# Kernel optimization log

Measured on AMD Instinct MI355X. Metric: run time of the kernel, lower is better.

## Reference

```python
import jax, jax.numpy as jnp
import numpy as np

EMBED = 512
HEADS = 8
HEAD_DIM = EMBED // HEADS
SCALE_BASE = 512
NEG = -1e9


def xpos_apply(x, offset, downscale):
    # x: [(b h), L, d]
    L, d = x.shape[1], x.shape[2]
    min_pos = -(L + offset) // 2
    max_pos = L + offset + min_pos
    base = (jnp.arange(0, d, 2, dtype=jnp.float32) + 0.4 * d) / (1.4 * d)      # [d/2]
    power = jnp.arange(min_pos, max_pos, dtype=jnp.float32) / SCALE_BASE        # [L']
    scale = base[None, :] ** power[:, None]                                     # [L', d/2]
    half = d // 2
    inv_freq = 1.0 / (10000.0 ** (jnp.arange(half, dtype=jnp.float32) / half))
    sinusoid = jnp.arange(scale.shape[0], dtype=jnp.float32)[:, None] * inv_freq[None, :]
    sin, cos = jnp.sin(sinusoid), jnp.cos(sinusoid)
    # keep last L rows (no-op when offset == 0)
    scale, sin, cos = scale[-L:], sin[-L:], cos[-L:]
    if downscale:
        scale = 1.0 / scale
    sin2 = jnp.repeat(sin * scale, 2, axis=-1)   # duplicate_interleave -> [L, d]
    cos2 = jnp.repeat(cos * scale, 2, axis=-1)
    x1, x2 = x[..., ::2], x[..., 1::2]
    rot = jnp.stack([-x2, x1], axis=-1).reshape(x.shape)  # rotate_every_two
    return x * cos2[None] + rot * sin2[None]


def split_heads(x, b, L):
    # 'b l (h d) -> (b h) l d'
    return x.reshape(b, L, HEADS, HEAD_DIM).transpose(0, 2, 1, 3).reshape(b * HEADS, L, HEAD_DIM)


def setup_inputs() -> dict:
    key = jax.random.key(0)
    ks = jax.random.split(key, 12)
    b, L = 4, 2048
    inp = {
        'query': jax.random.normal(ks[0], (b, L, EMBED), jnp.float32),
        'key': jax.random.normal(ks[1], (b, L, EMBED), jnp.float32),
        'value': jax.random.normal(ks[2], (b, L, EMBED), jnp.float32),
        'key_padding_mask': jnp.zeros((b, L), jnp.bool_),
        'attn_mask': jnp.where(jnp.tril(jnp.ones((L, L), jnp.bool_)), 0.0, NEG).astype(jnp.float32),
    }
    s = 1.0 / np.sqrt(EMBED)
    inp['Wq'] = jax.random.normal(ks[3], (EMBED, EMBED), jnp.float32) * s
    inp['bq'] = jnp.zeros((EMBED,), jnp.float32)
    inp['Wk'] = jax.random.normal(ks[4], (EMBED, EMBED), jnp.float32) * s
    inp['bk'] = jnp.zeros((EMBED,), jnp.float32)
    inp['Wv'] = jax.random.normal(ks[5], (EMBED, EMBED), jnp.float32) * s
    inp['bv'] = jnp.zeros((EMBED,), jnp.float32)
    inp['Wo'] = jax.random.normal(ks[6], (EMBED, EMBED), jnp.float32) * s
    inp['bo'] = jnp.zeros((EMBED,), jnp.float32)
    return inp


def reference(query, key, value, key_padding_mask, attn_mask, Wq, bq, Wk, bk, Wv, bv, Wo, bo):
    b, L, _ = query.shape
    q = split_heads(query @ Wq.T + bq, b, L)
    k = split_heads(key @ Wk.T + bk, b, L)
    v = split_heads(value @ Wv.T + bv, b, L)
    k = xpos_apply(k, 0, True)
    q = xpos_apply(q, 0, False)
    q = q * (HEAD_DIM ** -0.5)
    aw = jnp.einsum('btd,bsd->bts', q, k)                 # [(b h), t, s]
    aw = jnp.nan_to_num(aw) + attn_mask[None]
    aw = aw.reshape(b, HEADS, L, L)
    aw = jnp.where(key_padding_mask[:, None, None, :], jnp.finfo(aw.dtype).min, aw)
    aw = aw.reshape(b * HEADS, L, L)
    probs = jax.nn.softmax(aw.astype(jnp.float32), axis=-1).astype(aw.dtype)
    attn = jnp.einsum('bts,bsd->btd', probs, v)           # [(b h), t, d]
    attn = attn.reshape(b, HEADS, L, HEAD_DIM).transpose(0, 2, 1, 3).reshape(b, L, EMBED)
    return attn @ Wo.T + bo
```

## Files before the change

### kernel.cpp

```cpp
#include <hip/hip_runtime.h>
#include <hip/hip_bf16.h>

typedef __bf16 bf16x2 __attribute__((ext_vector_type(2)));
typedef __bf16 bf16x4 __attribute__((ext_vector_type(4)));
typedef __bf16 bf16x8 __attribute__((ext_vector_type(8)));
typedef float  f32x4  __attribute__((ext_vector_type(4)));

#define SEQ    2048
#define EMB    512
#define NHEAD  8
#define HD     64
#define NBATCH 4
#define MROWS  (NBATCH*SEQ)
#define QSCALE 0.18033688011112042f
#define INV2PI 0.15915494309189535f
#define TWOPI  6.28318530717958648f
#define NEGFREQ (-0.41524101186092028f)

__device__ __forceinline__ f32x4 mfma16(bf16x8 a, bf16x8 b, f32x4 c) {
  return __builtin_amdgcn_mfma_f32_16x16x32_bf16(a, b, c, 0, 0, 0);
}

typedef __attribute__((address_space(1))) const void gv_t;
typedef __attribute__((address_space(3))) void lv_t;
__device__ __forceinline__ void async16(const void* g, void* l) {
  __builtin_amdgcn_global_load_lds((gv_t*)g, (lv_t*)l, 16, 0, 0);
}

__global__ __launch_bounds__(256) void conv_kernel(const float* __restrict__ q,
                                                   const float* __restrict__ k,
                                                   const float* __restrict__ v,
                                                   __bf16* __restrict__ Qf,
                                                   __bf16* __restrict__ Kf,
                                                   __bf16* __restrict__ Vf) {
  const int z = blockIdx.y;
  const float* src = (z == 0) ? q : (z == 1) ? k : v;
  __bf16* dst = (z == 0) ? Qf : (z == 1) ? Kf : Vf;
  const size_t i8 = ((size_t)blockIdx.x * 256 + threadIdx.x) * 8;
  const float4 fa = ((const float4*)(src + i8))[0];
  const float4 fb = ((const float4*)(src + i8))[1];
  bf16x8 h = { (__bf16)fa.x, (__bf16)fa.y, (__bf16)fa.z, (__bf16)fa.w,
               (__bf16)fb.x, (__bf16)fb.y, (__bf16)fb.z, (__bf16)fb.w };
  *(bf16x8*)(dst + i8) = h;
}

__global__ __launch_bounds__(256) void convw_kernel(const float* __restrict__ wq,
                                                    const float* __restrict__ wk,
                                                    const float* __restrict__ wv,
                                                    const float* __restrict__ wo,
                                                    __bf16* __restrict__ Wb) {
  const int z = blockIdx.x >> 7;
  const float* src = (z == 0) ? wq : (z == 1) ? wk : (z == 2) ? wv : wo;
  __bf16* dst = Wb + (size_t)z * (EMB * EMB);
  const size_t i8 = ((size_t)(blockIdx.x & 127) * 256 + threadIdx.x) * 8;
  const float4 fa = ((const float4*)(src + i8))[0];
  const float4 fb = ((const float4*)(src + i8))[1];
  bf16x8 h = { (__bf16)fa.x, (__bf16)fa.y, (__bf16)fa.z, (__bf16)fa.w,
               (__bf16)fb.x, (__bf16)fb.y, (__bf16)fb.z, (__bf16)fb.w };
  *(bf16x8*)(dst + i8) = h;
}

__device__ __forceinline__ void gemm_main(const __bf16* __restrict__ A,
                                          const __bf16* __restrict__ W,
                                          __bf16* As, __bf16* Bs,
                                          f32x4 (&acc)[4][4], int m0, int n0) {
  const int tid = threadIdx.x;
  const int wid = tid >> 6, lane = tid & 63;
  const int quad = lane >> 4, l16 = lane & 15;
  const int l7 = l16 & 7;
  const int srow = lane >> 3;
  const int sxor = ((lane & 7) ^ srow) * 8;
  const int wm = (wid >> 1) * 64, wn = (wid & 1) * 64;

  #pragma unroll
  for (int i = 0; i < 4; ++i)
    #pragma unroll
    for (int j = 0; j < 4; ++j) acc[i][j] = (f32x4)(0.0f);

  for (int k0 = 0; k0 < 512; k0 += 64) {
    __syncthreads();
    #pragma unroll
    for (int ii = 0; ii < 4; ++ii) {
      const int r8 = wid * 32 + ii * 8;
      async16(A + (size_t)(m0 + r8 + srow) * 512 + k0 + sxor, &As[r8 * 64]);
      async16(W + (size_t)(n0 + r8 + srow) * 512 + k0 + sxor, &Bs[r8 * 64]);
    }
    __syncthreads();
    #pragma unroll
    for (int ks = 0; ks < 2; ++ks) {
      bf16x8 af[4], bfr[4];
      #pragma unroll
      for (int i = 0; i < 4; ++i)
        af[i] = *(const bf16x8*)&As[(wm + i * 16 + l16) * 64 +
                                    (((quad + ks * 4) ^ l7) * 8)];
      #pragma unroll
      for (int j = 0; j < 4; ++j)
        bfr[j] = *(const bf16x8*)&Bs[(wn + j * 16 + l16) * 64 +
                                     (((quad + ks * 4) ^ l7) * 8)];
      #pragma unroll
      for (int i = 0; i < 4; ++i)
        #pragma unroll
        for (int j = 0; j < 4; ++j)
          acc[i][j] = mfma16(af[i], bfr[j], acc[i][j]);
    }
  }
}

__global__ __launch_bounds__(256) void gemm_proj_kernel(
    const __bf16* __restrict__ Qf, const __bf16* __restrict__ Kf, const __bf16* __restrict__ Vf,
    const __bf16* __restrict__ Wb,
    const float* __restrict__ bq, const float* __restrict__ bk, const float* __restrict__ bv,
    __bf16* __restrict__ Qx, __bf16* __restrict__ Kx, __bf16* __restrict__ Vt) {
  __shared__ __align__(16) char smem[34816];
  __bf16* As = (__bf16*)smem;
  __bf16* Bs = (__bf16*)(smem + 16384);
  __bf16* T  = (__bf16*)smem;

  const int z = blockIdx.z;
  const __bf16* A = (z == 0) ? Qf : (z == 1) ? Kf : Vf;
  const __bf16* W = Wb + (size_t)z * (EMB * EMB);
  const float* bias = (z == 0) ? bq : (z == 1) ? bk : bv;
  const int m0 = blockIdx.y * 128, n0 = blockIdx.x * 128;

  f32x4 acc[4][4];
  gemm_main(A, W, As, Bs, acc, m0, n0);

  const int tid = threadIdx.x;
  const int wid = tid >> 6, lane = tid & 63;
  const int quad = lane >> 4, l16 = lane & 15;
  const int wm = (wid >> 1) * 64, wn = (wid & 1) * 64;

  __syncthreads();

  if (z == 2) {
    #pragma unroll
    for (int j = 0; j < 4; ++j) {
      const float bval = bias[n0 + wn + j * 16 + l16];
      #pragma unroll
      for (int i = 0; i < 4; ++i) {
        bf16x4 p = { (__bf16)(acc[i][j][0] + bval), (__bf16)(acc[i][j][1] + bval),
                     (__bf16)(acc[i][j][2] + bval), (__bf16)(acc[i][j][3] + bval) };
        *(bf16x4*)&T[(wn + j * 16 + l16) * 136 + wm + i * 16 + quad * 4] = p;
      }
    }
    __syncthreads();
    const int nrow = tid >> 1, mh = (tid & 1) << 6;
    bf16x8 vv[8];
    #pragma unroll
    for (int u = 0; u < 8; ++u) vv[u] = *(const bf16x8*)&T[nrow * 136 + mh + u * 8];
    const int n = n0 + nrow, h = n >> 6, d = n & 63;
    const int bb = m0 >> 11, lb2 = (m0 & 2047) + mh;
    __bf16* dst = Vt + ((size_t)(bb * 8 + h) * 64 + d) * 2048 + lb2;
    #pragma unroll
    for (int u = 0; u < 8; ++u) *(bf16x8*)(dst + u * 8) = vv[u];
  } else {
    #pragma unroll
    for (int j = 0; j < 4; ++j) {
      const float bval = bias[n0 + wn + j * 16 + l16];
      #pragma unroll
      for (int i = 0; i < 4; ++i)
        #pragma unroll
        for (int r = 0; r < 4; ++r)
          T[(wm + i * 16 + quad * 4 + r) * 136 + wn + j * 16 + l16] =
              (__bf16)(acc[i][j][r] + bval);
    }
    __syncthreads();
    const int lrow = tid >> 1, half = tid & 1;
    const int gm = m0 + lrow, l = gm & 2047, bb = gm >> 11;
    const int h = (n0 >> 6) + half;
    bf16x8 vv[8];
    #pragma unroll
    for (int u = 0; u < 8; ++u)
      vv[u] = *(const bf16x8*)&T[lrow * 136 + half * 64 + u * 8];
    bf16x8 ov[8];
    const float lf = (float)l;
    const float pw = (lf - 1024.0f) * (1.0f / 512.0f);
    const float qs = (z == 0) ? QSCALE : 1.0f;
    #pragma unroll
    for (int i = 0; i < 32; ++i) {
      const float x1 = (float)vv[i >> 2][(2 * i) & 7];
      const float x2 = (float)vv[i >> 2][(2 * i + 1) & 7];
      const float lb = __log2f((2.0f * i + 25.6f) * (1.0f / 89.6f));
      const float e  = (z == 0) ? (pw * lb) : (-pw * lb);
      const float sc = __builtin_amdgcn_exp2f(e) * qs;
      const float ang = lf * __builtin_amdgcn_exp2f((float)i * NEGFREQ);
      float rev = ang * INV2PI;
      rev -= floorf(rev);
      const float ar = rev * TWOPI;
      const float sn = __sinf(ar) * sc;
      const float cs = __cosf(ar) * sc;
      ov[i >> 2][(2 * i) & 7]     = (__bf16)(x1 * cs - x2 * sn);
      ov[i >> 2][(2 * i + 1) & 7] = (__bf16)(x2 * cs + x1 * sn);
    }
    __bf16* dst = ((z == 0) ? Qx : Kx) + ((size_t)(bb * 8 + h) * 2048 + l) * 64;
    #pragma unroll
    for (int u = 0; u < 8; ++u) *(bf16x8*)(dst + u * 8) = ov[u];
  }
}

__global__ __launch_bounds__(256) void gemm_out_kernel(
    const __bf16* __restrict__ A, const __bf16* __restrict__ W,
    const float* __restrict__ bias, float* __restrict__ C) {
  __shared__ __align__(16) char smem[34816];
  __bf16* As = (__bf16*)smem;
  __bf16* Bs = (__bf16*)(smem + 16384);
  const int m0 = blockIdx.y * 128, n0 = blockIdx.x * 128;
  f32x4 acc[4][4];
  gemm_main(A, W, As, Bs, acc, m0, n0);
  const int tid = threadIdx.x;
  const int wid = tid >> 6, lane = tid & 63;
  const int quad = lane >> 4, l16 = lane & 15;
  const int wm = (wid >> 1) * 64, wn = (wid & 1) * 64;
  #pragma unroll
  for (int j = 0; j < 4; ++j) {
    const int n = n0 + wn + j * 16 + l16;
    const float bval = bias[n];
    #pragma unroll
    for (int i = 0; i < 4; ++i)
      #pragma unroll
      for (int r = 0; r < 4; ++r)
        C[(size_t)(m0 + wm + i * 16 + quad * 4 + r) * 512 + n] = acc[i][j][r] + bval;
  }
}

__global__ __launch_bounds__(256) void flash_kernel(const __bf16* __restrict__ Qx,
                                                    const __bf16* __restrict__ Kx,
                                                    const __bf16* __restrict__ Vt,
                                                    const unsigned char* __restrict__ kpm,
                                                    __bf16* __restrict__ Oa) {
  __shared__ __align__(16) __bf16 Ks[2][64 * HD];
  __shared__ __align__(16) __bf16 Vs[2][64 * HD];
  __shared__ __align__(16) __bf16 Qs[64 * HD];

  const int tid = threadIdx.x;
  const int wid = tid >> 6;
  const int lane = tid & 63;
  const int quad = lane >> 4;
  const int l16 = lane & 15;
  const int l7 = l16 & 7;
  const int srow = lane >> 3;
  const int sxor = ((lane & 7) ^ srow) * 8;
  const int bh = blockIdx.x;
  const int b = bh >> 3;
  const int qb = 31 - (int)blockIdx.y;
  const int q0 = qb * 64;

  const __bf16* Qbase = Qx + (size_t)bh * (SEQ * HD);
  const __bf16* Kbase = Kx + (size_t)bh * (SEQ * HD);
  const __bf16* Vbase = Vt + (size_t)bh * (HD * SEQ);
  __bf16* Pw = Qs + wid * 1024;

  #pragma unroll
  for (int ii = 0; ii < 2; ++ii) {
    const int r0 = wid * 16 + ii * 8;
    async16(Qbase + (size_t)(q0 + r0 + srow) * HD + sxor, &Qs[r0 * HD]);
    async16(Kbase + (size_t)(r0 + srow) * HD + sxor, &Ks[0][r0 * HD]);
    async16(Vbase + (size_t)(r0 + srow) * SEQ + sxor, &Vs[0][r0 * HD]);
  }
  __syncthreads();
  const bf16x8 qf0 = *(const bf16x8*)&Qs[(wid * 16 + l16) * HD + ((quad ^ l7) * 8)];
  const bf16x8 qf1 = *(const bf16x8*)&Qs[(wid * 16 + l16) * HD + (((quad + 4) ^ l7) * 8)];

  f32x4 o0 = (f32x4)(0.0f), o1 = (f32x4)(0.0f), o2 = (f32x4)(0.0f), o3 = (f32x4)(0.0f);
  float m_run = -1e30f, l_run = 0.0f;
  const int myq = q0 + wid * 16 + l16;
  const int niter = qb + 1;

  for (int it = 0; it < niter; ++it) {
    const int kv0 = it << 6;
    const int cur = it & 1;
    const __bf16* Kc = &Ks[cur][0];
    const __bf16* Vc = &Vs[cur][0];

    if (it + 1 < niter) {
      const int kn = kv0 + 64;
      #pragma unroll
      for (int ii = 0; ii < 2; ++ii) {
        const int r0 = wid * 16 + ii * 8;
        async16(Kbase + (size_t)(kn + r0 + srow) * HD + sxor, &Ks[cur ^ 1][r0 * HD]);
        async16(Vbase + (size_t)(r0 + srow) * SEQ + kn + sxor, &Vs[cur ^ 1][r0 * HD]);
      }
    }
    const unsigned char* kp0 = kpm + b * SEQ + kv0;
    unsigned pk[4];
    #pragma unroll
    for (int nb = 0; nb < 4; ++nb)
      pk[nb] = *(const unsigned*)(kp0 + nb * 16 + quad * 4);

    f32x4 s[4];
    #pragma unroll
    for (int nb = 0; nb < 4; ++nb) s[nb] = (f32x4)(0.0f);
    __builtin_amdgcn_s_setprio(1);
    #pragma unroll
    for (int nb = 0; nb < 4; ++nb) {
      const bf16x8 kf = *(const bf16x8*)&Kc[(nb * 16 + l16) * HD + ((quad ^ l7) * 8)];
      s[nb] = mfma16(kf, qf0, s[nb]);
    }
    #pragma unroll
    for (int nb = 0; nb < 4; ++nb) {
      const bf16x8 kf = *(const bf16x8*)&Kc[(nb * 16 + l16) * HD + (((quad + 4) ^ l7) * 8)];
      s[nb] = mfma16(kf, qf1, s[nb]);
    }
    __builtin_amdgcn_s_setprio(0);

    if (kv0 + 63 > q0 + wid * 16) {
      #pragma unroll
      for (int nb = 0; nb < 4; ++nb)
        #pragma unroll
        for (int r = 0; r < 4; ++r)
          if (kv0 + nb * 16 + quad * 4 + r > myq) s[nb][r] = -1e30f;
    }
    #pragma unroll
    for (int nb = 0; nb < 4; ++nb) {
      if (pk[nb]) {
        if (pk[nb] & 0x000000FFu) s[nb][0] = -1e30f;
        if (pk[nb] & 0x0000FF00u) s[nb][1] = -1e30f;
        if (pk[nb] & 0x00FF0000u) s[nb][2] = -1e30f;
        if (pk[nb] & 0xFF000000u) s[nb][3] = -1e30f;
      }
    }

    float mx;
    {
      f32x4 u0, u1;
      #pragma unroll
      for (int r = 0; r < 4; ++r) u0[r] = fmaxf(s[0][r], s[1][r]);
      #pragma unroll
      for (int r = 0; r < 4; ++r) u1[r] = fmaxf(s[2][r], s[3][r]);
      #pragma unroll
      for (int r = 0; r < 4; ++r) u0[r] = fmaxf(u0[r], u1[r]);
      mx = fmaxf(fmaxf(u0[0], u0[1]), fmaxf(u0[2], u0[3]));
    }
    mx = fmaxf(mx, __shfl_xor(mx, 16));
    mx = fmaxf(mx, __shfl_xor(mx, 32));
    if (__any(mx > m_run)) {
      const float m_new = fmaxf(m_run, mx);
      const float alpha = __builtin_amdgcn_exp2f(m_run - m_new);
      o0 *= alpha; o1 *= alpha; o2 *= alpha; o3 *= alpha;
      l_run *= alpha;
      m_run = m_new;
    }
    #pragma unroll
    for (int nb = 0; nb < 4; ++nb)
      #pragma unroll
      for (int r = 0; r < 4; ++r)
        s[nb][r] = __builtin_amdgcn_exp2f(s[nb][r] - m_run);
    {
      f32x4 v01 = s[0] + s[1];
      f32x4 v23 = s[2] + s[3];
      f32x4 vt = v01 + v23;
      float ssum = (vt[0] + vt[1]) + (vt[2] + vt[3]);
      ssum += __shfl_xor(ssum, 16);
      ssum += __shfl_xor(ssum, 32);
      l_run += ssum;
    }

    #pragma unroll
    for (int nb = 0; nb < 4; ++nb) {
      bf16x4 p4 = { (__bf16)s[nb][0], (__bf16)s[nb][1],
                    (__bf16)s[nb][2], (__bf16)s[nb][3] };
      *(bf16x4*)&Pw[l16 * 64 + (((nb * 2 + (quad >> 1)) ^ l7) << 3) + (quad & 1) * 4] = p4;
    }

    __builtin_amdgcn_s_setprio(1);
    #pragma unroll
    for (int ks = 0; ks < 2; ++ks) {
      const bf16x8 pf = *(const bf16x8*)&Pw[l16 * 64 + (((ks * 4 + quad) ^ l7) << 3)];
      const int bx = ((quad + ks * 4) ^ l7) * 8;
      o0 = mfma16(*(const bf16x8*)&Vc[( 0 + l16) * HD + bx], pf, o0);
      o1 = mfma16(*(const bf16x8*)&Vc[(16 + l16) * HD + bx], pf, o1);
      o2 = mfma16(*(const bf16x8*)&Vc[(32 + l16) * HD + bx], pf, o2);
      o3 = mfma16(*(const bf16x8*)&Vc[(48 + l16) * HD + bx], pf, o3);
    }
    __builtin_amdgcn_s_setprio(0);

    if (it + 1 < niter) __syncthreads();
  }

  const float inv_l = 1.0f / l_run;
  {
    bf16x4 t0 = { (__bf16)(o0[0] * inv_l), (__bf16)(o0[1] * inv_l),
                  (__bf16)(o0[2] * inv_l), (__bf16)(o0[3] * inv_l) };
    bf16x4 t1 = { (__bf16)(o1[0] * inv_l), (__bf16)(o1[1] * inv_l),
                  (__bf16)(o1[2] * inv_l), (__bf16)(o1[3] * inv_l) };
    bf16x4 t2 = { (__bf16)(o2[0] * inv_l), (__bf16)(o2[1] * inv_l),
                  (__bf16)(o2[2] * inv_l), (__bf16)(o2[3] * inv_l) };
    bf16x4 t3 = { (__bf16)(o3[0] * inv_l), (__bf16)(o3[1] * inv_l),
                  (__bf16)(o3[2] * inv_l), (__bf16)(o3[3] * inv_l) };
    *(bf16x4*)&Pw[l16 * 64 + (((0 + (quad >> 1)) ^ l7) << 3) + (quad & 1) * 4] = t0;
    *(bf16x4*)&Pw[l16 * 64 + (((2 + (quad >> 1)) ^ l7) << 3) + (quad & 1) * 4] = t1;
    *(bf16x4*)&Pw[l16 * 64 + (((4 + (quad >> 1)) ^ l7) << 3) + (quad & 1) * 4] = t2;
    *(bf16x4*)&Pw[l16 * 64 + (((6 + (quad >> 1)) ^ l7) << 3) + (quad & 1) * 4] = t3;
  }
  const int h = bh & 7;
  #pragma unroll
  for (int ii = 0; ii < 2; ++ii) {
    const int qr = ii * 8 + (lane >> 3);
    const bf16x8 ovv = *(const bf16x8*)&Pw[qr * 64 + (((lane & 7) ^ (qr & 7)) << 3)];
    *(bf16x8*)(Oa + (((size_t)b * SEQ + q0 + wid * 16 + qr) * NHEAD + h) * HD +
               (lane & 7) * 8) = ovv;
  }
}

extern "C" void kernel_launch(void* const* d_in, const int* in_sizes, int n_in,
                              void* d_out, int out_size, void* d_ws, size_t ws_size,
                              hipStream_t stream) {
  (void)in_sizes; (void)n_in; (void)out_size; (void)ws_size;
  const float* query = (const float*)d_in[0];
  const float* key   = (const float*)d_in[1];
  const float* value = (const float*)d_in[2];
  const unsigned char* kpm = (const unsigned char*)d_in[3];
  const float* Wq = (const float*)d_in[5];
  const float* bq = (const float*)d_in[6];
  const float* Wk = (const float*)d_in[7];
  const float* bk = (const float*)d_in[8];
  const float* Wv = (const float*)d_in[9];
  const float* bv = (const float*)d_in[10];
  const float* Wo = (const float*)d_in[11];
  const float* bo = (const float*)d_in[12];
  float* out = (float*)d_out;

  char* ws = (char*)d_ws;
  const size_t SZ = (size_t)MROWS * EMB * 2;
  __bf16* Qf = (__bf16*)(ws);
  __bf16* Kf = (__bf16*)(ws + SZ);
  __bf16* Vf = (__bf16*)(ws + 2 * SZ);
  __bf16* Qx = (__bf16*)(ws + 3 * SZ);
  __bf16* Kx = (__bf16*)(ws + 4 * SZ);
  __bf16* Vt = (__bf16*)(ws + 5 * SZ);
  __bf16* Wb = (__bf16*)(ws + 6 * SZ);
  __bf16* Oa = Qf;

  conv_kernel<<<dim3(2048, 3), dim3(256), 0, stream>>>(query, key, value, Qf, Kf, Vf);
  convw_kernel<<<dim3(512), dim3(256), 0, stream>>>(Wq, Wk, Wv, Wo, Wb);
  gemm_proj_kernel<<<dim3(4, 64, 3), dim3(256), 0, stream>>>(
      Qf, Kf, Vf, Wb, bq, bk, bv, Qx, Kx, Vt);
  flash_kernel<<<dim3(32, 32), dim3(256), 0, stream>>>(Qx, Kx, Vt, kpm, Oa);
  gemm_out_kernel<<<dim3(4, 64), dim3(256), 0, stream>>>(
      Oa, Wb + (size_t)3 * EMB * EMB, bo, out);
}
```

Baseline: 213.2 us.

## Split long causal query tiles across two blocks and merge with combine kernel

The flash kernel now splits the 16 longest causal query tiles per head into two KV halves, so 1536 blocks with more balanced work replace 1024 uneven ones. Each half writes unnormalised fp32 partial outputs and m/l stats to scratch, and a new combine kernel rescales, merges and transposes them into the attention output. The change also merges the two fp32-to-bf16 conversion launches into one, skips the padding-mask loads unless any key is masked, and moves the row max/sum shuffles off the common path. In exchange it adds an extra launch, scratch traffic and reuse of the Kf and out buffers as temporary storage.

```diff
diff --git a/kernel.cpp b/kernel.cpp
--- a/kernel.cpp
+++ b/kernel.cpp
@@ -30,29 +30,29 @@
 __global__ __launch_bounds__(256) void conv_kernel(const float* __restrict__ q,
                                                    const float* __restrict__ k,
                                                    const float* __restrict__ v,
+                                                   const float* __restrict__ wq,
+                                                   const float* __restrict__ wk,
+                                                   const float* __restrict__ wv,
+                                                   const float* __restrict__ wo,
                                                    __bf16* __restrict__ Qf,
                                                    __bf16* __restrict__ Kf,
-                                                   __bf16* __restrict__ Vf) {
+                                                   __bf16* __restrict__ Vf,
+                                                   __bf16* __restrict__ Wb) {
   const int z = blockIdx.y;
-  const float* src = (z == 0) ? q : (z == 1) ? k : v;
-  __bf16* dst = (z == 0) ? Qf : (z == 1) ? Kf : Vf;
-  const size_t i8 = ((size_t)blockIdx.x * 256 + threadIdx.x) * 8;
-  const float4 fa = ((const float4*)(src + i8))[0];
-  const float4 fb = ((const float4*)(src + i8))[1];
-  bf16x8 h = { (__bf16)fa.x, (__bf16)fa.y, (__bf16)fa.z, (__bf16)fa.w,
-               (__bf16)fb.x, (__bf16)fb.y, (__bf16)fb.z, (__bf16)fb.w };
-  *(bf16x8*)(dst + i8) = h;
-}
-
-__global__ __launch_bounds__(256) void convw_kernel(const float* __restrict__ wq,
-                                                    const float* __restrict__ wk,
-                                                    const float* __restrict__ wv,
-                                                    const float* __restrict__ wo,
-                                                    __bf16* __restrict__ Wb) {
-  const int z = blockIdx.x >> 7;
-  const float* src = (z == 0) ? wq : (z == 1) ? wk : (z == 2) ? wv : wo;
-  __bf16* dst = Wb + (size_t)z * (EMB * EMB);
-  const size_t i8 = ((size_t)(blockIdx.x & 127) * 256 + threadIdx.x) * 8;
+  const float* src;
+  __bf16* dst;
+  size_t i8;
+  if (z < 3) {
+    src = (z == 0) ? q : (z == 1) ? k : v;
+    dst = (z == 0) ? Qf : (z == 1) ? Kf : Vf;
+    i8 = ((size_t)blockIdx.x * 256 + threadIdx.x) * 8;
+  } else {
+    if (blockIdx.x >= 512) return;
+    const int zw = blockIdx.x >> 7;
+    src = (zw == 0) ? wq : (zw == 1) ? wk : (zw == 2) ? wv : wo;
+    dst = Wb + (size_t)zw * (EMB * EMB);
+    i8 = ((size_t)(blockIdx.x & 127) * 256 + threadIdx.x) * 8;
+  }
   const float4 fa = ((const float4*)(src + i8))[0];
   const float4 fb = ((const float4*)(src + i8))[1];
   bf16x8 h = { (__bf16)fa.x, (__bf16)fa.y, (__bf16)fa.z, (__bf16)fa.w,
@@ -227,7 +227,9 @@
                                                     const __bf16* __restrict__ Kx,
                                                     const __bf16* __restrict__ Vt,
                                                     const unsigned char* __restrict__ kpm,
-                                                    __bf16* __restrict__ Oa) {
+                                                    __bf16* __restrict__ Oa,
+                                                    float* __restrict__ PartO,
+                                                    float* __restrict__ Pml) {
   __shared__ __align__(16) __bf16 Ks[2][64 * HD];
   __shared__ __align__(16) __bf16 Vs[2][64 * HD];
   __shared__ __align__(16) __bf16 Qs[64 * HD];
@@ -242,7 +244,20 @@
   const int sxor = ((lane & 7) ^ srow) * 8;
   const int bh = blockIdx.x;
   const int b = bh >> 3;
-  const int qb = 31 - (int)blockIdx.y;
+  const int y = blockIdx.y;
+
+  int qb, it0, it1, split;
+  if (y < 32) {
+    qb = 31 - (y >> 1);
+    split = 1;
+    const int nt = qb + 1, hh = nt >> 1;
+    if ((y & 1) == 0) { it0 = 0;  it1 = hh; }
+    else              { it0 = hh; it1 = nt; }
+  } else {
+    qb = 47 - y;
+    split = 0;
+    it0 = 0; it1 = qb + 1;
+  }
   const int q0 = qb * 64;
 
   const __bf16* Qbase = Qx + (size_t)bh * (SEQ * HD);
@@ -254,25 +269,26 @@
   for (int ii = 0; ii < 2; ++ii) {
     const int r0 = wid * 16 + ii * 8;
     async16(Qbase + (size_t)(q0 + r0 + srow) * HD + sxor, &Qs[r0 * HD]);
-    async16(Kbase + (size_t)(r0 + srow) * HD + sxor, &Ks[0][r0 * HD]);
-    async16(Vbase + (size_t)(r0 + srow) * SEQ + sxor, &Vs[0][r0 * HD]);
+    async16(Kbase + (size_t)(it0 * 64 + r0 + srow) * HD + sxor, &Ks[0][r0 * HD]);
+    async16(Vbase + (size_t)(r0 + srow) * SEQ + it0 * 64 + sxor, &Vs[0][r0 * HD]);
   }
   __syncthreads();
   const bf16x8 qf0 = *(const bf16x8*)&Qs[(wid * 16 + l16) * HD + ((quad ^ l7) * 8)];
   const bf16x8 qf1 = *(const bf16x8*)&Qs[(wid * 16 + l16) * HD + (((quad + 4) ^ l7) * 8)];
 
-  f32x4 o0 = (f32x4)(0.0f), o1 = (f32x4)(0.0f), o2 = (f32x4)(0.0f), o3 = (f32x4)(0.0f);
+  f32x4 o[4];
+  #pragma unroll
+  for (int i = 0; i < 4; ++i) o[i] = (f32x4)(0.0f);
   float m_run = -1e30f, l_run = 0.0f;
   const int myq = q0 + wid * 16 + l16;
-  const int niter = qb + 1;
-
-  for (int it = 0; it < niter; ++it) {
+
+  for (int it = it0; it < it1; ++it) {
     const int kv0 = it << 6;
-    const int cur = it & 1;
+    const int cur = (it - it0) & 1;
     const __bf16* Kc = &Ks[cur][0];
     const __bf16* Vc = &Vs[cur][0];
 
-    if (it + 1 < niter) {
+    if (it + 1 < it1) {
       const int kn = kv0 + 64;
       #pragma unroll
       for (int ii = 0; ii < 2; ++ii) {
@@ -281,11 +297,8 @@
         async16(Vbase + (size_t)(r0 + srow) * SEQ + kn + sxor, &Vs[cur ^ 1][r0 * HD]);
       }
     }
-    const unsigned char* kp0 = kpm + b * SEQ + kv0;
-    unsigned pk[4];
-    #pragma unroll
-    for (int nb = 0; nb < 4; ++nb)
-      pk[nb] = *(const unsigned*)(kp0 + nb * 16 + quad * 4);
+    const unsigned mine =
+        *(const unsigned*)(kpm + b * SEQ + kv0 + ((lane & 15) << 2));
 
     f32x4 s[4];
     #pragma unroll
@@ -310,13 +323,17 @@
         for (int r = 0; r < 4; ++r)
           if (kv0 + nb * 16 + quad * 4 + r > myq) s[nb][r] = -1e30f;
     }
-    #pragma unroll
-    for (int nb = 0; nb < 4; ++nb) {
-      if (pk[nb]) {
-        if (pk[nb] & 0x000000FFu) s[nb][0] = -1e30f;
-        if (pk[nb] & 0x0000FF00u) s[nb][1] = -1e30f;
-        if (pk[nb] & 0x00FF0000u) s[nb][2] = -1e30f;
-        if (pk[nb] & 0xFF000000u) s[nb][3] = -1e30f;
+    if (__any(mine != 0)) {
+      const unsigned char* kp0 = kpm + b * SEQ + kv0;
+      #pragma unroll
+      for (int nb = 0; nb < 4; ++nb) {
+        const unsigned pk = *(const unsigned*)(kp0 + nb * 16 + quad * 4);
+        if (pk) {
+          if (pk & 0x000000FFu) s[nb][0] = -1e30f;
+          if (pk & 0x0000FF00u) s[nb][1] = -1e30f;
+          if (pk & 0x00FF0000u) s[nb][2] = -1e30f;
+          if (pk & 0xFF000000u) s[nb][3] = -1e30f;
+        }
       }
     }
 
@@ -331,12 +348,13 @@
       for (int r = 0; r < 4; ++r) u0[r] = fmaxf(u0[r], u1[r]);
       mx = fmaxf(fmaxf(u0[0], u0[1]), fmaxf(u0[2], u0[3]));
     }
-    mx = fmaxf(mx, __shfl_xor(mx, 16));
-    mx = fmaxf(mx, __shfl_xor(mx, 32));
     if (__any(mx > m_run)) {
-      const float m_new = fmaxf(m_run, mx);
+      float rm = fmaxf(mx, __shfl_xor(mx, 16));
+      rm = fmaxf(rm, __shfl_xor(rm, 32));
+      const float m_new = fmaxf(m_run, rm);
       const float alpha = __builtin_amdgcn_exp2f(m_run - m_new);
-      o0 *= alpha; o1 *= alpha; o2 *= alpha; o3 *= alpha;
+      #pragma unroll
+      for (int i = 0; i < 4; ++i) o[i] *= alpha;
       l_run *= alpha;
       m_run = m_new;
     }
@@ -349,10 +367,7 @@
       f32x4 v01 = s[0] + s[1];
       f32x4 v23 = s[2] + s[3];
       f32x4 vt = v01 + v23;
-      float ssum = (vt[0] + vt[1]) + (vt[2] + vt[3]);
-      ssum += __shfl_xor(ssum, 16);
-      ssum += __shfl_xor(ssum, 32);
-      l_run += ssum;
+      l_run += (vt[0] + vt[1]) + (vt[2] + vt[3]);
     }
 
     #pragma unroll
@@ -367,26 +382,43 @@
     for (int ks = 0; ks < 2; ++ks) {
       const bf16x8 pf = *(const bf16x8*)&Pw[l16 * 64 + (((ks * 4 + quad) ^ l7) << 3)];
       const int bx = ((quad + ks * 4) ^ l7) * 8;
-      o0 = mfma16(*(const bf16x8*)&Vc[( 0 + l16) * HD + bx], pf, o0);
-      o1 = mfma16(*(const bf16x8*)&Vc[(16 + l16) * HD + bx], pf, o1);
-      o2 = mfma16(*(const bf16x8*)&Vc[(32 + l16) * HD + bx], pf, o2);
-      o3 = mfma16(*(const bf16x8*)&Vc[(48 + l16) * HD + bx], pf, o3);
+      #pragma unroll
+      for (int j = 0; j < 4; ++j)
+        o[j] = mfma16(*(const bf16x8*)&Vc[(j * 16 + l16) * HD + bx], pf, o[j]);
     }
     __builtin_amdgcn_s_setprio(0);
 
-    if (it + 1 < niter) __syncthreads();
-  }
-
-  const float inv_l = 1.0f / l_run;
+    if (it + 1 < it1) __syncthreads();
+  }
+
+  float lt = l_run + __shfl_xor(l_run, 16);
+  lt += __shfl_xor(lt, 32);
+
+  if (split) {
+    const int tile = (bh * 16 + (qb - 16)) * 2 + (y & 1);
+    float* po = PartO + (size_t)tile * 4096;
+    #pragma unroll
+    for (int i = 0; i < 4; ++i)
+      #pragma unroll
+      for (int r = 0; r < 4; ++r)
+        po[(i * 16 + quad * 4 + r) * 64 + wid * 16 + l16] = o[i][r];
+    if (quad == 0) {
+      Pml[(size_t)tile * 128 + wid * 16 + l16] = m_run;
+      Pml[(size_t)tile * 128 + 64 + wid * 16 + l16] = lt;
+    }
+    return;
+  }
+
+  const float inv_l = 1.0f / lt;
   {
-    bf16x4 t0 = { (__bf16)(o0[0] * inv_l), (__bf16)(o0[1] * inv_l),
-                  (__bf16)(o0[2] * inv_l), (__bf16)(o0[3] * inv_l) };
-    bf16x4 t1 = { (__bf16)(o1[0] * inv_l), (__bf16)(o1[1] * inv_l),
-                  (__bf16)(o1[2] * inv_l), (__bf16)(o1[3] * inv_l) };
-    bf16x4 t2 = { (__bf16)(o2[0] * inv_l), (__bf16)(o2[1] * inv_l),
-                  (__bf16)(o2[2] * inv_l), (__bf16)(o2[3] * inv_l) };
-    bf16x4 t3 = { (__bf16)(o3[0] * inv_l), (__bf16)(o3[1] * inv_l),
-                  (__bf16)(o3[2] * inv_l), (__bf16)(o3[3] * inv_l) };
+    bf16x4 t0 = { (__bf16)(o[0][0] * inv_l), (__bf16)(o[0][1] * inv_l),
+                  (__bf16)(o[0][2] * inv_l), (__bf16)(o[0][3] * inv_l) };
+    bf16x4 t1 = { (__bf16)(o[1][0] * inv_l), (__bf16)(o[1][1] * inv_l),
+                  (__bf16)(o[1][2] * inv_l), (__bf16)(o[1][3] * inv_l) };
+    bf16x4 t2 = { (__bf16)(o[2][0] * inv_l), (__bf16)(o[2][1] * inv_l),
+                  (__bf16)(o[2][2] * inv_l), (__bf16)(o[2][3] * inv_l) };
+    bf16x4 t3 = { (__bf16)(o[3][0] * inv_l), (__bf16)(o[3][1] * inv_l),
+                  (__bf16)(o[3][2] * inv_l), (__bf16)(o[3][3] * inv_l) };
     *(bf16x4*)&Pw[l16 * 64 + (((0 + (quad >> 1)) ^ l7) << 3) + (quad & 1) * 4] = t0;
     *(bf16x4*)&Pw[l16 * 64 + (((2 + (quad >> 1)) ^ l7) << 3) + (quad & 1) * 4] = t1;
     *(bf16x4*)&Pw[l16 * 64 + (((4 + (quad >> 1)) ^ l7) << 3) + (quad & 1) * 4] = t2;
@@ -400,6 +432,45 @@
     *(bf16x8*)(Oa + (((size_t)b * SEQ + q0 + wid * 16 + qr) * NHEAD + h) * HD +
                (lane & 7) * 8) = ovv;
   }
+}
+
+__global__ __launch_bounds__(256) void combine_kernel(const float* __restrict__ PartO,
+                                                      const float* __restrict__ Pml,
+                                                      __bf16* __restrict__ Oa) {
+  __shared__ __align__(16) __bf16 T[64 * 72];
+  const int pair = blockIdx.x;
+  const int bh = pair >> 4, qb = 16 + (pair & 15);
+  const int b = bh >> 3, h = bh & 7, q0 = qb * 64;
+  const float* P0 = PartO + (size_t)pair * 2 * 4096;
+  const float* P1 = P0 + 4096;
+  const float* ml = Pml + (size_t)pair * 2 * 128;
+  const int t = threadIdx.x;
+  const int d = t >> 2, qg = (t & 3) * 16;
+
+  float w0[16], w1[16];
+  #pragma unroll
+  for (int k = 0; k < 16; ++k) {
+    const float m0 = ml[qg + k],       l0 = ml[64 + qg + k];
+    const float m1 = ml[128 + qg + k], l1 = ml[192 + qg + k];
+    const float m = fmaxf(m0, m1);
+    const float a0 = __builtin_amdgcn_exp2f(m0 - m);
+    const float a1 = __builtin_amdgcn_exp2f(m1 - m);
+    const float inv = 1.0f / (a0 * l0 + a1 * l1);
+    w0[k] = a0 * inv;
+    w1[k] = a1 * inv;
+  }
+  #pragma unroll
+  for (int k = 0; k < 16; ++k) {
+    const float v = P0[d * 64 + qg + k] * w0[k] + P1[d * 64 + qg + k] * w1[k];
+    T[(qg + k) * 72 + d] = (__bf16)v;
+  }
+  __syncthreads();
+  const int q = t >> 2, dg = (t & 3) * 16;
+  const bf16x8 va = *(const bf16x8*)&T[q * 72 + dg];
+  const bf16x8 vb = *(const bf16x8*)&T[q * 72 + dg + 8];
+  __bf16* dst = Oa + (((size_t)b * SEQ + q0 + q) * NHEAD + h) * HD + dg;
+  *(bf16x8*)dst = va;
+  *(bf16x8*)(dst + 8) = vb;
 }
 
 extern "C" void kernel_launch(void* const* d_in, const int* in_sizes, int n_in,
@@ -430,12 +501,16 @@
   __bf16* Vt = (__bf16*)(ws + 5 * SZ);
   __bf16* Wb = (__bf16*)(ws + 6 * SZ);
   __bf16* Oa = Qf;
-
-  conv_kernel<<<dim3(2048, 3), dim3(256), 0, stream>>>(query, key, value, Qf, Kf, Vf);
-  convw_kernel<<<dim3(512), dim3(256), 0, stream>>>(Wq, Wk, Wv, Wo, Wb);
+  float* PartO = (float*)(ws + SZ);
+  float* Pml = out;
+
+  conv_kernel<<<dim3(2048, 4), dim3(256), 0, stream>>>(
+      query, key, value, Wq, Wk, Wv, Wo, Qf, Kf, Vf, Wb);
   gemm_proj_kernel<<<dim3(4, 64, 3), dim3(256), 0, stream>>>(
       Qf, Kf, Vf, Wb, bq, bk, bv, Qx, Kx, Vt);
-  flash_kernel<<<dim3(32, 32), dim3(256), 0, stream>>>(Qx, Kx, Vt, kpm, Oa);
+  flash_kernel<<<dim3(32, 48), dim3(256), 0, stream>>>(
+      Qx, Kx, Vt, kpm, Oa, PartO, Pml);
+  combine_kernel<<<dim3(512), dim3(256), 0, stream>>>(PartO, Pml, Oa);
   gemm_out_kernel<<<dim3(4, 64), dim3(256), 0, stream>>>(
       Oa, Wb + (size_t)3 * EMB * EMB, bo, out);
 }
```

Result: slower. 221.9 us (+4.0%).
